# Kernel optimization log

Measured on AMD Instinct MI355X. Metric: run time of the kernel, lower is better.

Reference implementation:

```python
import jax, jax.numpy as jnp
import numpy as np

V, E, H = 32000, 256, 512  # vocab, embedding_size, hidden_size
B, T = 64, 512             # batch, seq_len


def setup_inputs() -> dict:
    key = jax.random.key(0)
    ks = jax.random.split(key, 8)
    inputs = jax.random.randint(ks[0], (B, T), 0, V)
    lengths = jax.random.randint(ks[1], (B,), 0, T)
    reset_indices = jax.random.randint(ks[2], (B, T), 0, 2, dtype=jnp.int32)
    # nn.Embedding: N(0,1) init with padding_idx row zeroed
    emb = jax.random.normal(ks[3], (V, E), dtype=jnp.float32).at[0].set(0.0)
    # nn.LSTMCell params: uniform(-1/sqrt(H), 1/sqrt(H)), gate order i,f,g,o
    s = 1.0 / np.sqrt(H)
    W_ih = jax.random.uniform(ks[4], (4 * H, E), minval=-s, maxval=s, dtype=jnp.float32)
    W_hh = jax.random.uniform(ks[5], (4 * H, H), minval=-s, maxval=s, dtype=jnp.float32)
    b_ih = jax.random.uniform(ks[6], (4 * H,), minval=-s, maxval=s, dtype=jnp.float32)
    b_hh = jax.random.uniform(ks[7], (4 * H,), minval=-s, maxval=s, dtype=jnp.float32)
    return {"inputs": inputs, "lengths": lengths, "reset_indices": reset_indices,
            "emb": emb, "W_ih": W_ih, "W_hh": W_hh, "b_ih": b_ih, "b_hh": b_hh}


def reference(inputs, lengths, reset_indices, emb, W_ih, W_hh, b_ih, b_hh):
    x = emb[inputs]                                        # (B,T,E); dropout is identity in eval
    mask = (jnp.arange(T) < lengths[:, None]).astype(x.dtype)   # (B,T) length mask
    xt = jnp.swapaxes(x, 0, 1)                             # (T,B,E) time-major
    m_t = mask.T                                           # (T,B)
    r_t = reset_indices.astype(x.dtype).T                  # (T,B)
    # precompute input contribution to gates for all timesteps
    gates_x = jnp.einsum('tbe,ge->tbg', xt, W_ih) + b_ih + b_hh  # (T,B,4H)

    def step(carry, inp):
        h, c = carry
        gx, m, r = inp
        g = gx + h @ W_hh.T                                # (B,4H)
        i, f, gg, o = jnp.split(g, 4, axis=-1)
        i = jax.nn.sigmoid(i); f = jax.nn.sigmoid(f)
        gg = jnp.tanh(gg); o = jax.nn.sigmoid(o)
        c_new = f * c + i * gg
        h_new = o * jnp.tanh(c_new)
        mm = m[:, None]; rr = r[:, None]
        h_next = h_new * mm + h * (1 - mm)                 # mask-blend (keep state past length)
        c_next = c_new * mm + c * (1 - mm)
        # reset zeroing applied to carried state AFTER output is recorded
        return (h_next * (1 - rr), c_next * (1 - rr)), h_next

    h0 = jnp.zeros((B, H), dtype=x.dtype)
    (hT, cT), out_t = jax.lax.scan(step, (h0, h0), (gates_x, m_t, r_t))  # out_t: (T,B,H)
    output = jnp.swapaxes(out_t, 0, 1)                     # (B,T,H) = output.transpose(0,1)
    return output, hT, cT, mask
```

## Files before the change

kernel.cpp:

```cpp
#include <hip/hip_runtime.h>
#include <stdint.h>
#include <stddef.h>

constexpr int V = 32000, E = 256, H = 512, B = 64, T = 512;
constexpr int NTHR = 512;
constexpr int NBLK = 64;
constexpr int BATG = 16;
constexpr int HPB = 32;

constexpr int PSW = 128 * 17;
constexpr int OFF_PS   = 0;
constexpr int OFF_BIAS = OFF_PS + 8 * PSW * 4;
constexpr int OFF_LEN  = OFF_BIAS + 128 * 4;
constexpr int LDS_BYTES = 84 * 1024;

constexpr size_t OUT_HT   = (size_t)B * T * H;
constexpr size_t OUT_CT   = OUT_HT + (size_t)B * H;
constexpr size_t OUT_MASK = OUT_CT + (size_t)B * H;

typedef __attribute__((ext_vector_type(8))) short short8;
typedef __attribute__((ext_vector_type(4))) float f32x4;
typedef __attribute__((ext_vector_type(4))) unsigned int u32x4;

__device__ __forceinline__ unsigned short f2bf(float f) {
  uint32_t u = __builtin_bit_cast(uint32_t, f);
  return (unsigned short)((u + 0x7fffu + ((u >> 16) & 1u)) >> 16);
}
__device__ __forceinline__ short8 pack_bf8(float4 v0, float4 v1) {
  short8 r;
  r[0] = (short)f2bf(v0.x); r[1] = (short)f2bf(v0.y);
  r[2] = (short)f2bf(v0.z); r[3] = (short)f2bf(v0.w);
  r[4] = (short)f2bf(v1.x); r[5] = (short)f2bf(v1.y);
  r[6] = (short)f2bf(v1.z); r[7] = (short)f2bf(v1.w);
  return r;
}
__device__ __forceinline__ float sigmoidf_fast(float x) {
  return 1.f / (1.f + __expf(-x));
}
__device__ __forceinline__ float tanhf_fast(float x) {
  return 1.f - 2.f / (__expf(2.f * x) + 1.f);
}
__device__ __forceinline__ void st_word(uint32_t* p, uint32_t v) {
  __hip_atomic_store(p, v, __ATOMIC_RELAXED, __HIP_MEMORY_SCOPE_AGENT);
}
__device__ __forceinline__ void ld_mall_4x4(const uint32_t* p, u32x4& r0,
                                            u32x4& r1, u32x4& r2, u32x4& r3) {
  asm volatile(
      "global_load_dwordx4 %0, %4, off sc1\n\t"
      "global_load_dwordx4 %1, %4, off offset:64 sc1\n\t"
      "global_load_dwordx4 %2, %4, off offset:128 sc1\n\t"
      "global_load_dwordx4 %3, %4, off offset:192 sc1\n\t"
      "s_waitcnt vmcnt(0)"
      : "=&v"(r0), "=&v"(r1), "=&v"(r2), "=&v"(r3)
      : "v"(p)
      : "memory");
}

__global__ void __launch_bounds__(NTHR, 1)
lstm_mfma(const int* __restrict__ inputs, const int* __restrict__ lengths,
          const int* __restrict__ resets, const float* __restrict__ emb,
          const float* __restrict__ W_ih, const float* __restrict__ W_hh,
          const float* __restrict__ b_ih, const float* __restrict__ b_hh,
          float* __restrict__ out, int* __restrict__ ctr,
          uint32_t* __restrict__ hw) {
  extern __shared__ char lds[];
  float* Ps = (float*)(lds + OFF_PS);
  float* Bias = (float*)(lds + OFF_BIAS);
  int* Lens = (int*)(lds + OFF_LEN);

  const int tid = threadIdx.x;
  const int blk = blockIdx.x;
  const int grp = blk & 3;
  const int rq = blk >> 2;
  const int khid = rq * HPB;
  const int b0 = grp * BATG;
  int* flags = ctr + grp * 64;

  const int w = tid >> 6;
  const int L = tid & 63;
  const int lc = L & 15;
  const int q = L >> 4;

  short8 wf[4][8];
  if (w < 4) {
    #pragma unroll
    for (int s = 0; s < 4; ++s) {
      #pragma unroll
      for (int tl = 0; tl < 8; ++tl) {
        const int n = 16 * tl + lc;
        const int grow = (n >> 5) * H + khid + (n & 31);
        const float* src = W_hh + (size_t)grow * H + 128 * w + 32 * s + 8 * q;
        wf[s][tl] = pack_bf8(*(const float4*)src, *(const float4*)(src + 4));
      }
    }
  } else {
    #pragma unroll
    for (int s = 0; s < 2; ++s) {
      #pragma unroll
      for (int tl = 0; tl < 8; ++tl) {
        const int n = 16 * tl + lc;
        const int grow = (n >> 5) * H + khid + (n & 31);
        const float* src = W_ih + (size_t)grow * E + 64 * (w - 4) + 32 * s + 8 * q;
        wf[s][tl] = pack_bf8(*(const float4*)src, *(const float4*)(src + 4));
      }
    }
  }
  if (tid < 128) {
    const int grow = (tid >> 5) * H + khid + (tid & 31);
    Bias[tid] = b_ih[grow] + b_hh[grow];
  }
  if (tid < 16) Lens[tid] = lengths[b0 + tid];
  {
    int i = blk * 512 + tid;
    int mb = i >> 9, mt = i & (T - 1);
    out[OUT_MASK + i] = (mt < lengths[mb]) ? 1.f : 0.f;
  }
  __syncthreads();

  const int jj = tid & 31;
  const int bb = tid >> 5;

  float carry_h = 0.f, carry_c = 0.f;

  for (int t = 0; t < T; ++t) {
    const uint32_t* hsrc = hw + (size_t)(t & 1) * (B * 256);
    uint32_t* hdst = hw + (size_t)((t + 1) & 1) * (B * 256);

    float rr = (float)resets[(b0 + bb) * T + t];
    f32x4 acc[8];
    #pragma unroll
    for (int tl = 0; tl < 8; ++tl) acc[tl] = (f32x4){0.f, 0.f, 0.f, 0.f};

    if (w >= 4) {
      const int tok = inputs[(b0 + lc) * T + t];
      const float* eb = emb + (size_t)tok * E + 64 * (w - 4) + 8 * q;
      short8 a0 = pack_bf8(*(const float4*)eb, *(const float4*)(eb + 4));
      short8 a1 = pack_bf8(*(const float4*)(eb + 32), *(const float4*)(eb + 36));
      #pragma unroll
      for (int tl = 0; tl < 8; ++tl)
        acc[tl] = __builtin_amdgcn_mfma_f32_16x16x32_bf16(a0, wf[0][tl], acc[tl], 0, 0, 0);
      #pragma unroll
      for (int tl = 0; tl < 8; ++tl)
        acc[tl] = __builtin_amdgcn_mfma_f32_16x16x32_bf16(a1, wf[1][tl], acc[tl], 0, 0, 0);
    }

    if (t > 0) {
      if (w == 0) {
        for (;;) {
          int v = 0x7fffffff;
          if (L < 16) v = __hip_atomic_load(&flags[L], __ATOMIC_RELAXED,
                                            __HIP_MEMORY_SCOPE_AGENT);
          if (__all(v >= t)) break;
          __builtin_amdgcn_s_sleep(1);
        }
      }
      __syncthreads();
      if (w < 4) {
        const uint32_t* p = hsrc + (size_t)(b0 + lc) * 256 + 64 * w + 4 * q;
        u32x4 r0, r1, r2, r3;
        ld_mall_4x4(p, r0, r1, r2, r3);
        short8 a0 = __builtin_bit_cast(short8, r0);
        short8 a1 = __builtin_bit_cast(short8, r1);
        short8 a2 = __builtin_bit_cast(short8, r2);
        short8 a3 = __builtin_bit_cast(short8, r3);
        #pragma unroll
        for (int tl = 0; tl < 8; ++tl)
          acc[tl] = __builtin_amdgcn_mfma_f32_16x16x32_bf16(a0, wf[0][tl], acc[tl], 0, 0, 0);
        #pragma unroll
        for (int tl = 0; tl < 8; ++tl)
          acc[tl] = __builtin_amdgcn_mfma_f32_16x16x32_bf16(a1, wf[1][tl], acc[tl], 0, 0, 0);
        #pragma unroll
        for (int tl = 0; tl < 8; ++tl)
          acc[tl] = __builtin_amdgcn_mfma_f32_16x16x32_bf16(a2, wf[2][tl], acc[tl], 0, 0, 0);
        #pragma unroll
        for (int tl = 0; tl < 8; ++tl)
          acc[tl] = __builtin_amdgcn_mfma_f32_16x16x32_bf16(a3, wf[3][tl], acc[tl], 0, 0, 0);
      }
    }

    #pragma unroll
    for (int tl = 0; tl < 8; ++tl)
      *(f32x4*)(Ps + w * PSW + (16 * tl + lc) * 17 + 4 * q) = acc[tl];
    __syncthreads();

    float g4[4];
    #pragma unroll
    for (int gi = 0; gi < 4; ++gi) {
      const int n = gi * 32 + jj;
      float s = Bias[n];
      #pragma unroll
      for (int ww = 0; ww < 8; ++ww) s += Ps[ww * PSW + n * 17 + bb];
      g4[gi] = s;
    }
    float ig = sigmoidf_fast(g4[0]);
    float fg = sigmoidf_fast(g4[1]);
    float gg = tanhf_fast(g4[2]);
    float og = sigmoidf_fast(g4[3]);
    float c_new = fg * carry_c + ig * gg;
    float h_new = og * tanhf_fast(c_new);
    bool live = (t < Lens[bb]);
    float h_next = live ? h_new : carry_h;
    float c_next = live ? c_new : carry_c;
    carry_h = h_next * (1.f - rr);
    carry_c = c_next * (1.f - rr);

    float ph = __shfl(carry_h, L ^ 1);
    if (t < T - 1) {
      if ((tid & 1) == 0) {
        uint32_t word = (uint32_t)f2bf(carry_h) | ((uint32_t)f2bf(ph) << 16);
        st_word(hdst + (size_t)(b0 + bb) * 256 + 16 * rq + (jj >> 1), word);
      }
      __syncthreads();
      if (tid == 0)
        __hip_atomic_store(&flags[rq], t + 1, __ATOMIC_RELAXED,
                           __HIP_MEMORY_SCOPE_AGENT);
    }
    out[((size_t)(b0 + bb) * T + t) * H + khid + jj] = h_next;
  }
  out[OUT_HT + (size_t)(b0 + bb) * H + khid + jj] = carry_h;
  out[OUT_CT + (size_t)(b0 + bb) * H + khid + jj] = carry_c;
}

extern "C" void kernel_launch(void* const* d_in, const int* in_sizes, int n_in,
                              void* d_out, int out_size, void* d_ws, size_t ws_size,
                              hipStream_t stream) {
  const int* inputs    = (const int*)d_in[0];
  const int* lengths   = (const int*)d_in[1];
  const int* resets    = (const int*)d_in[2];
  const float* emb     = (const float*)d_in[3];
  const float* W_ih    = (const float*)d_in[4];
  const float* W_hh    = (const float*)d_in[5];
  const float* b_ih    = (const float*)d_in[6];
  const float* b_hh    = (const float*)d_in[7];
  float* out = (float*)d_out;

  int* ctr = (int*)d_ws;
  uint32_t* hw = (uint32_t*)((char*)d_ws + 4096);

  hipFuncSetAttribute((const void*)lstm_mfma,
                      hipFuncAttributeMaxDynamicSharedMemorySize, LDS_BYTES);

  hipMemsetAsync(d_ws, 0, 4096, stream);
  lstm_mfma<<<NBLK, NTHR, LDS_BYTES, stream>>>(
      inputs, lengths, resets, emb, W_ih, W_hh, b_ih, b_hh, out, ctr, hw);
}
```

Measured before the change: 2.051 ms.

## Replace flag-based grid sync with tagged h-state words polled per wave

Removes the per-group flag counters and block-wide barrier wait. Each h value is now written as fp32 with a sequence tag in its low 3 mantissa bits, and every consumer wave spins directly on the data until all tags match the expected step. The K dimension is also rebalanced so all 8 waves each do one embedding MFMA and two recurrent MFMAs, instead of waves 0-3 doing recurrence and 4-7 doing embedding. This trades a flag round-trip and barrier for larger fp32 traffic, on-device bf16 conversion, and a small precision loss from the tag bits.

```diff
diff --git a/kernel.cpp b/kernel.cpp
--- a/kernel.cpp
+++ b/kernel.cpp
@@ -43,17 +43,26 @@
 __device__ __forceinline__ void st_word(uint32_t* p, uint32_t v) {
   __hip_atomic_store(p, v, __ATOMIC_RELAXED, __HIP_MEMORY_SCOPE_AGENT);
 }
-__device__ __forceinline__ void ld_mall_4x4(const uint32_t* p, u32x4& r0,
+__device__ __forceinline__ void ld_mall_k64(const uint32_t* p, u32x4& r0,
                                             u32x4& r1, u32x4& r2, u32x4& r3) {
   asm volatile(
       "global_load_dwordx4 %0, %4, off sc1\n\t"
-      "global_load_dwordx4 %1, %4, off offset:64 sc1\n\t"
+      "global_load_dwordx4 %1, %4, off offset:16 sc1\n\t"
       "global_load_dwordx4 %2, %4, off offset:128 sc1\n\t"
-      "global_load_dwordx4 %3, %4, off offset:192 sc1\n\t"
+      "global_load_dwordx4 %3, %4, off offset:144 sc1\n\t"
       "s_waitcnt vmcnt(0)"
       : "=&v"(r0), "=&v"(r1), "=&v"(r2), "=&v"(r3)
       : "v"(p)
       : "memory");
+}
+__device__ __forceinline__ short8 cvt_frag(u32x4 lo, u32x4 hi) {
+  uint32_t d0, d1, d2, d3;
+  asm("v_cvt_pk_bf16_f32 %0, %1, %2" : "=v"(d0) : "v"(lo[0]), "v"(lo[1]));
+  asm("v_cvt_pk_bf16_f32 %0, %1, %2" : "=v"(d1) : "v"(lo[2]), "v"(lo[3]));
+  asm("v_cvt_pk_bf16_f32 %0, %1, %2" : "=v"(d2) : "v"(hi[0]), "v"(hi[1]));
+  asm("v_cvt_pk_bf16_f32 %0, %1, %2" : "=v"(d3) : "v"(hi[2]), "v"(hi[3]));
+  u32x4 d = {d0, d1, d2, d3};
+  return __builtin_bit_cast(short8, d);
 }
 
 __global__ void __launch_bounds__(NTHR, 1)
@@ -61,8 +70,7 @@
           const int* __restrict__ resets, const float* __restrict__ emb,
           const float* __restrict__ W_ih, const float* __restrict__ W_hh,
           const float* __restrict__ b_ih, const float* __restrict__ b_hh,
-          float* __restrict__ out, int* __restrict__ ctr,
-          uint32_t* __restrict__ hw) {
+          float* __restrict__ out, uint32_t* __restrict__ hw) {
   extern __shared__ char lds[];
   float* Ps = (float*)(lds + OFF_PS);
   float* Bias = (float*)(lds + OFF_BIAS);
@@ -74,36 +82,30 @@
   const int rq = blk >> 2;
   const int khid = rq * HPB;
   const int b0 = grp * BATG;
-  int* flags = ctr + grp * 64;
 
   const int w = tid >> 6;
   const int L = tid & 63;
   const int lc = L & 15;
   const int q = L >> 4;
 
-  short8 wf[4][8];
-  if (w < 4) {
-    #pragma unroll
-    for (int s = 0; s < 4; ++s) {
-      #pragma unroll
-      for (int tl = 0; tl < 8; ++tl) {
-        const int n = 16 * tl + lc;
-        const int grow = (n >> 5) * H + khid + (n & 31);
-        const float* src = W_hh + (size_t)grow * H + 128 * w + 32 * s + 8 * q;
-        wf[s][tl] = pack_bf8(*(const float4*)src, *(const float4*)(src + 4));
-      }
-    }
-  } else {
-    #pragma unroll
-    for (int s = 0; s < 2; ++s) {
-      #pragma unroll
-      for (int tl = 0; tl < 8; ++tl) {
-        const int n = 16 * tl + lc;
-        const int grow = (n >> 5) * H + khid + (n & 31);
-        const float* src = W_ih + (size_t)grow * E + 64 * (w - 4) + 32 * s + 8 * q;
-        wf[s][tl] = pack_bf8(*(const float4*)src, *(const float4*)(src + 4));
-      }
-    }
+  short8 wfh[2][8];
+  short8 wfe[8];
+  #pragma unroll
+  for (int s = 0; s < 2; ++s) {
+    #pragma unroll
+    for (int tl = 0; tl < 8; ++tl) {
+      const int n = 16 * tl + lc;
+      const int grow = (n >> 5) * H + khid + (n & 31);
+      const float* src = W_hh + (size_t)grow * H + 64 * w + 32 * s + 8 * q;
+      wfh[s][tl] = pack_bf8(*(const float4*)src, *(const float4*)(src + 4));
+    }
+  }
+  #pragma unroll
+  for (int tl = 0; tl < 8; ++tl) {
+    const int n = 16 * tl + lc;
+    const int grow = (n >> 5) * H + khid + (n & 31);
+    const float* src = W_ih + (size_t)grow * E + 32 * w + 8 * q;
+    wfe[tl] = pack_bf8(*(const float4*)src, *(const float4*)(src + 4));
   }
   if (tid < 128) {
     const int grow = (tid >> 5) * H + khid + (tid & 31);
@@ -123,59 +125,44 @@
   float carry_h = 0.f, carry_c = 0.f;
 
   for (int t = 0; t < T; ++t) {
-    const uint32_t* hsrc = hw + (size_t)(t & 1) * (B * 256);
-    uint32_t* hdst = hw + (size_t)((t + 1) & 1) * (B * 256);
+    const uint32_t* hsrc = hw + (size_t)(t & 1) * (B * H);
+    uint32_t* hdst = hw + (size_t)((t + 1) & 1) * (B * H);
 
     float rr = (float)resets[(b0 + bb) * T + t];
+    const int tok = inputs[(b0 + lc) * T + t];
+    const float* eb = emb + (size_t)tok * E + 32 * w + 8 * q;
+    short8 ae = pack_bf8(*(const float4*)eb, *(const float4*)(eb + 4));
     f32x4 acc[8];
-    #pragma unroll
-    for (int tl = 0; tl < 8; ++tl) acc[tl] = (f32x4){0.f, 0.f, 0.f, 0.f};
-
-    if (w >= 4) {
-      const int tok = inputs[(b0 + lc) * T + t];
-      const float* eb = emb + (size_t)tok * E + 64 * (w - 4) + 8 * q;
-      short8 a0 = pack_bf8(*(const float4*)eb, *(const float4*)(eb + 4));
-      short8 a1 = pack_bf8(*(const float4*)(eb + 32), *(const float4*)(eb + 36));
+    const f32x4 zero4 = {0.f, 0.f, 0.f, 0.f};
+    #pragma unroll
+    for (int tl = 0; tl < 8; ++tl)
+      acc[tl] = __builtin_amdgcn_mfma_f32_16x16x32_bf16(ae, wfe[tl], zero4, 0, 0, 0);
+
+    if (t > 0) {
+      const uint32_t expect = 4u | (((uint32_t)(t - 1) >> 1) & 3u);
+      const uint32_t* p = hsrc + (size_t)(b0 + lc) * H + 64 * w + 8 * q;
+      u32x4 r0, r1, r2, r3;
+      for (;;) {
+        ld_mall_k64(p, r0, r1, r2, r3);
+        uint32_t o = (r0[0] | r0[1] | r0[2] | r0[3]) |
+                     (r1[0] | r1[1] | r1[2] | r1[3]) |
+                     (r2[0] | r2[1] | r2[2] | r2[3]) |
+                     (r3[0] | r3[1] | r3[2] | r3[3]);
+        uint32_t a = (r0[0] & r0[1] & r0[2] & r0[3]) &
+                     (r1[0] & r1[1] & r1[2] & r1[3]) &
+                     (r2[0] & r2[1] & r2[2] & r2[3]) &
+                     (r3[0] & r3[1] & r3[2] & r3[3]);
+        uint32_t bad = ((o ^ expect) | (a ^ expect)) & 7u;
+        if (!__any((int)bad)) break;
+      }
+      short8 a0 = cvt_frag(r0, r1);
+      short8 a1 = cvt_frag(r2, r3);
       #pragma unroll
       for (int tl = 0; tl < 8; ++tl)
-        acc[tl] = __builtin_amdgcn_mfma_f32_16x16x32_bf16(a0, wf[0][tl], acc[tl], 0, 0, 0);
+        acc[tl] = __builtin_amdgcn_mfma_f32_16x16x32_bf16(a0, wfh[0][tl], acc[tl], 0, 0, 0);
       #pragma unroll
       for (int tl = 0; tl < 8; ++tl)
-        acc[tl] = __builtin_amdgcn_mfma_f32_16x16x32_bf16(a1, wf[1][tl], acc[tl], 0, 0, 0);
-    }
-
-    if (t > 0) {
-      if (w == 0) {
-        for (;;) {
-          int v = 0x7fffffff;
-          if (L < 16) v = __hip_atomic_load(&flags[L], __ATOMIC_RELAXED,
-                                            __HIP_MEMORY_SCOPE_AGENT);
-          if (__all(v >= t)) break;
-          __builtin_amdgcn_s_sleep(1);
-        }
-      }
-      __syncthreads();
-      if (w < 4) {
-        const uint32_t* p = hsrc + (size_t)(b0 + lc) * 256 + 64 * w + 4 * q;
-        u32x4 r0, r1, r2, r3;
-        ld_mall_4x4(p, r0, r1, r2, r3);
-        short8 a0 = __builtin_bit_cast(short8, r0);
-        short8 a1 = __builtin_bit_cast(short8, r1);
-        short8 a2 = __builtin_bit_cast(short8, r2);
-        short8 a3 = __builtin_bit_cast(short8, r3);
-        #pragma unroll
-        for (int tl = 0; tl < 8; ++tl)
-          acc[tl] = __builtin_amdgcn_mfma_f32_16x16x32_bf16(a0, wf[0][tl], acc[tl], 0, 0, 0);
-        #pragma unroll
-        for (int tl = 0; tl < 8; ++tl)
-          acc[tl] = __builtin_amdgcn_mfma_f32_16x16x32_bf16(a1, wf[1][tl], acc[tl], 0, 0, 0);
-        #pragma unroll
-        for (int tl = 0; tl < 8; ++tl)
-          acc[tl] = __builtin_amdgcn_mfma_f32_16x16x32_bf16(a2, wf[2][tl], acc[tl], 0, 0, 0);
-        #pragma unroll
-        for (int tl = 0; tl < 8; ++tl)
-          acc[tl] = __builtin_amdgcn_mfma_f32_16x16x32_bf16(a3, wf[3][tl], acc[tl], 0, 0, 0);
-      }
+        acc[tl] = __builtin_amdgcn_mfma_f32_16x16x32_bf16(a1, wfh[1][tl], acc[tl], 0, 0, 0);
     }
 
     #pragma unroll
@@ -192,6 +179,8 @@
       for (int ww = 0; ww < 8; ++ww) s += Ps[ww * PSW + n * 17 + bb];
       g4[gi] = s;
     }
+    __syncthreads();
+
     float ig = sigmoidf_fast(g4[0]);
     float fg = sigmoidf_fast(g4[1]);
     float gg = tanhf_fast(g4[2]);
@@ -204,16 +193,10 @@
     carry_h = h_next * (1.f - rr);
     carry_c = c_next * (1.f - rr);
 
-    float ph = __shfl(carry_h, L ^ 1);
     if (t < T - 1) {
-      if ((tid & 1) == 0) {
-        uint32_t word = (uint32_t)f2bf(carry_h) | ((uint32_t)f2bf(ph) << 16);
-        st_word(hdst + (size_t)(b0 + bb) * 256 + 16 * rq + (jj >> 1), word);
-      }
-      __syncthreads();
-      if (tid == 0)
-        __hip_atomic_store(&flags[rq], t + 1, __ATOMIC_RELAXED,
-                           __HIP_MEMORY_SCOPE_AGENT);
+      const uint32_t wtag = 4u | (((uint32_t)t >> 1) & 3u);
+      uint32_t bits = (__builtin_bit_cast(uint32_t, carry_h) & ~7u) | wtag;
+      st_word(hdst + (size_t)(b0 + bb) * H + HPB * rq + jj, bits);
     }
     out[((size_t)(b0 + bb) * T + t) * H + khid + jj] = h_next;
   }
@@ -234,13 +217,12 @@
   const float* b_hh    = (const float*)d_in[7];
   float* out = (float*)d_out;
 
-  int* ctr = (int*)d_ws;
-  uint32_t* hw = (uint32_t*)((char*)d_ws + 4096);
+  uint32_t* hw = (uint32_t*)d_ws;
 
   hipFuncSetAttribute((const void*)lstm_mfma,
                       hipFuncAttributeMaxDynamicSharedMemorySize, LDS_BYTES);
 
-  hipMemsetAsync(d_ws, 0, 4096, stream);
+  hipMemsetAsync(d_ws, 0, (size_t)2 * B * H * 4, stream);
   lstm_mfma<<<NBLK, NTHR, LDS_BYTES, stream>>>(
-      inputs, lengths, resets, emb, W_ih, W_hh, b_ih, b_hh, out, ctr, hw);
-}
+      inputs, lengths, resets, emb, W_ih, W_hh, b_ih, b_hh, out, hw);
+}
```

Result: no change. 2.088 ms (+1.8%).
